# Optimization experiments

Measured on AMD Instinct MI355X. Metric: run time of the kernel, lower is better.

The kernel has to match this reference:

```python
import jax, jax.numpy as jnp
import numpy as np

EMBED = 768
HEADS = 12
HEAD_DIM = EMBED // HEADS
HIDDEN = 4 * EMBED
EPS = 1e-5


def _layernorm(x, g, b):
    mu = jnp.mean(x, axis=-1, keepdims=True)
    var = jnp.var(x, axis=-1, keepdims=True)
    return (x - mu) * jax.lax.rsqrt(var + EPS) * g + b


def setup_inputs() -> dict:
    key = jax.random.key(0)
    ks = jax.random.split(key, 12)
    s_e = 1.0 / np.sqrt(EMBED)
    s_h = 1.0 / np.sqrt(HIDDEN)
    return {
        "x": jax.random.normal(ks[0], (2, 2048, EMBED), dtype=jnp.float32),
        "ln1_g": jnp.ones((EMBED,), jnp.float32),
        "ln1_b": jnp.zeros((EMBED,), jnp.float32),
        "qkv_w": jax.random.uniform(ks[1], (EMBED, 3 * EMBED), jnp.float32, -s_e, s_e),
        "qkv_b": jax.random.uniform(ks[2], (3 * EMBED,), jnp.float32, -s_e, s_e),
        "proj_w": jax.random.uniform(ks[3], (EMBED, EMBED), jnp.float32, -s_e, s_e),
        "proj_b": jax.random.uniform(ks[4], (EMBED,), jnp.float32, -s_e, s_e),
        "ln2_g": jnp.ones((EMBED,), jnp.float32),
        "ln2_b": jnp.zeros((EMBED,), jnp.float32),
        "fc1_w": jax.random.uniform(ks[5], (EMBED, HIDDEN), jnp.float32, -s_e, s_e),
        "fc1_b": jax.random.uniform(ks[6], (HIDDEN,), jnp.float32, -s_e, s_e),
        "fc2_w": jax.random.uniform(ks[7], (HIDDEN, EMBED), jnp.float32, -s_h, s_h),
        "fc2_b": jax.random.uniform(ks[8], (EMBED,), jnp.float32, -s_h, s_h),
    }


def reference(x, ln1_g, ln1_b, qkv_w, qkv_b, proj_w, proj_b,
              ln2_g, ln2_b, fc1_w, fc1_b, fc2_w, fc2_b):
    B, L, C = x.shape
    scale = HEAD_DIM ** -0.5

    # --- attention sublayer (pre-LN) ---
    h = _layernorm(x, ln1_g, ln1_b)
    qkv = h @ qkv_w + qkv_b                       # [B, L, 3C]
    qkv = qkv.reshape(B, L, 3, HEADS, HEAD_DIM)
    q = jnp.transpose(qkv[:, :, 0], (0, 2, 1, 3))  # [B, H, L, D]
    k = jnp.transpose(qkv[:, :, 1], (0, 2, 1, 3))
    v = jnp.transpose(qkv[:, :, 2], (0, 2, 1, 3))
    attn = jnp.einsum('bhqd,bhkd->bhqk', q, k) * scale  # [B, H, L, L]
    attn = jax.nn.softmax(attn, axis=-1)
    out = jnp.einsum('bhqk,bhkd->bhqd', attn, v)  # [B, H, L, D]
    out = jnp.transpose(out, (0, 2, 1, 3)).reshape(B, L, C)
    x = x + (out @ proj_w + proj_b)

    # --- FFN sublayer (pre-LN) ---
    h = _layernorm(x, ln2_g, ln2_b)
    h = jax.nn.gelu(h @ fc1_w + fc1_b, approximate=False)
    x = x + (h @ fc2_w + fc2_b)
    return x
```

## Files before the change

kernel.cpp:

```cpp
#include <hip/hip_runtime.h>
#include <hip/hip_bf16.h>
#include <math.h>

#define EMBED   768
#define NHEADS  12
#define HD      64
#define HIDDEN  3072
#define SEQ     2048
#define BATCH   2
#define ROWS    (BATCH*SEQ)

#define QSCALE  0.1803368801111204f

typedef __bf16 bf16_t;
typedef __attribute__((ext_vector_type(8))) __bf16 bf16x8;
typedef __attribute__((ext_vector_type(4))) __bf16 bf16x4;
typedef __attribute__((ext_vector_type(4))) float f32x4;

static __device__ __forceinline__ f32x4 mfma16(bf16x8 a, bf16x8 b, f32x4 c) {
  return __builtin_amdgcn_mfma_f32_16x16x32_bf16(a, b, c, 0, 0, 0);
}

#if defined(__HIP_DEVICE_COMPILE__) && __has_builtin(__builtin_amdgcn_exp2f)
static __device__ __forceinline__ float fast_exp2(float x) {
  return __builtin_amdgcn_exp2f(x);
}
#else
static __device__ __forceinline__ float fast_exp2(float x) { return exp2f(x); }
#endif

#if defined(__HIP_DEVICE_COMPILE__) && __has_builtin(__builtin_amdgcn_rcpf)
static __device__ __forceinline__ float fast_rcp(float x) {
  return __builtin_amdgcn_rcpf(x);
}
#else
static __device__ __forceinline__ float fast_rcp(float x) { return 1.0f / x; }
#endif

typedef __attribute__((address_space(1))) const void gas_void;
typedef __attribute__((address_space(3))) void las_void;
static __device__ __forceinline__ void gll16(const void* g, void* l) {
  __builtin_amdgcn_global_load_lds((gas_void*)g, (las_void*)l, 16, 0, 0);
}

__global__ __launch_bounds__(256) void prep_kernel(
    const float* __restrict__ w0, bf16_t* __restrict__ o0,
    const float* __restrict__ w1, bf16_t* __restrict__ o1,
    const float* __restrict__ w2, bf16_t* __restrict__ o2,
    const float* __restrict__ w3, bf16_t* __restrict__ o3,
    const float* __restrict__ x,  const float* __restrict__ g,
    const float* __restrict__ bt, bf16_t* __restrict__ lnout)
{
  __shared__ float tile[32][33];
  __shared__ float red[8];
  int lin = blockIdx.x;
  if (lin < 6912) {
    const float* in; bf16_t* out; int R, C, bx, by;
    if (lin < 1728)      { in = w0; out = o0; R = 768;  C = 2304; bx = lin % 72; by = lin / 72; }
    else if (lin < 2304) { in = w1; out = o1; R = 768;  C = 768;  lin -= 1728; bx = lin % 24; by = lin / 24; }
    else if (lin < 4608) { in = w2; out = o2; R = 768;  C = 3072; lin -= 2304; bx = lin % 96; by = lin / 96; }
    else                 { in = w3; out = o3; R = 3072; C = 768;  lin -= 4608; bx = lin % 24; by = lin / 24; }
    int c0 = bx * 32, r0 = by * 32;
    int tx = threadIdx.x & 31, ty = threadIdx.x >> 5;
    #pragma unroll
    for (int p = 0; p < 4; ++p) {
      int r = ty + p * 8;
      tile[r][tx] = in[(size_t)(r0 + r) * C + c0 + tx];
    }
    __syncthreads();
    #pragma unroll
    for (int p = 0; p < 4; ++p) {
      int cc = ty + p * 8;
      out[(size_t)(c0 + cc) * R + r0 + tx] = (bf16_t)tile[tx][cc];
    }
    return;
  }
  int row = lin - 6912;
  int tid = threadIdx.x;
  const float* xr = x + (size_t)row * EMBED;
  float v0 = xr[tid], v1 = xr[tid + 256], v2 = xr[tid + 512];
  float s  = v0 + v1 + v2;
  float s2 = v0*v0 + v1*v1 + v2*v2;
  #pragma unroll
  for (int o = 32; o >= 1; o >>= 1) {
    s  += __shfl_xor(s,  o, 64);
    s2 += __shfl_xor(s2, o, 64);
  }
  int wave = tid >> 6, lane = tid & 63;
  if (lane == 0) { red[wave] = s; red[wave + 4] = s2; }
  __syncthreads();
  s  = red[0] + red[1] + red[2] + red[3];
  s2 = red[4] + red[5] + red[6] + red[7];
  float mu  = s * (1.0f / EMBED);
  float var = s2 * (1.0f / EMBED) - mu * mu;
  float rs  = rsqrtf(var + 1e-5f);
  bf16_t* orow = lnout + (size_t)row * EMBED;
  orow[tid]       = (bf16_t)((v0 - mu) * rs * g[tid]       + bt[tid]);
  orow[tid + 256] = (bf16_t)((v1 - mu) * rs * g[tid + 256] + bt[tid + 256]);
  orow[tid + 512] = (bf16_t)((v2 - mu) * rs * g[tid + 512] + bt[tid + 512]);
}

__global__ __launch_bounds__(256) void ln_kernel(
    const float* __restrict__ x, const float* __restrict__ g,
    const float* __restrict__ bt, bf16_t* __restrict__ out)
{
  int row = blockIdx.x;
  int tid = threadIdx.x;
  const float* xr = x + (size_t)row * EMBED;
  float v0 = xr[tid], v1 = xr[tid + 256], v2 = xr[tid + 512];
  float s  = v0 + v1 + v2;
  float s2 = v0*v0 + v1*v1 + v2*v2;
  #pragma unroll
  for (int o = 32; o >= 1; o >>= 1) {
    s  += __shfl_xor(s,  o, 64);
    s2 += __shfl_xor(s2, o, 64);
  }
  __shared__ float red[8];
  int wave = tid >> 6, lane = tid & 63;
  if (lane == 0) { red[wave] = s; red[wave + 4] = s2; }
  __syncthreads();
  s  = red[0] + red[1] + red[2] + red[3];
  s2 = red[4] + red[5] + red[6] + red[7];
  float mu  = s * (1.0f / EMBED);
  float var = s2 * (1.0f / EMBED) - mu * mu;
  float rs  = rsqrtf(var + 1e-5f);
  bf16_t* orow = out + (size_t)row * EMBED;
  orow[tid]       = (bf16_t)((v0 - mu) * rs * g[tid]       + bt[tid]);
  orow[tid + 256] = (bf16_t)((v1 - mu) * rs * g[tid + 256] + bt[tid + 256]);
  orow[tid + 512] = (bf16_t)((v2 - mu) * rs * g[tid + 512] + bt[tid + 512]);
}

template<int MODE, int BN, int SK = 1>
__global__ __launch_bounds__(256) void gemm_kernel(
    const bf16_t* __restrict__ A, const bf16_t* __restrict__ WT,
    const float* __restrict__ bias, const float* __restrict__ res,
    void* __restrict__ outp, bf16_t* __restrict__ vt, int N, int K)
{
  constexpr int JT = BN / 32;
  __shared__ bf16_t As[128 * 64];
  __shared__ bf16_t Bs[BN * 64];
  int tid = threadIdx.x;
  int lane = tid & 63, wave = tid >> 6;
  int l15 = lane & 15, quad = lane >> 4;
  int wm = wave >> 1, wn = wave & 1;

  int Nn = N / BN;
  int lin = blockIdx.x;
  int kslice = 0, k_lo = 0, k_hi = K;
  if (MODE == 4) {
    kslice = lin % SK; lin /= SK;
    k_lo = kslice * (K / SK); k_hi = k_lo + K / SK;
  }
  int bm = (lin & 7) + 8 * ((lin >> 3) / Nn);
  int bn = (lin >> 3) % Nn;
  int m0 = bm * 128, n0 = bn * BN;

  f32x4 acc[4][JT];
  #pragma unroll
  for (int i = 0; i < 4; ++i)
    #pragma unroll
    for (int j = 0; j < JT; ++j)
      acc[i][j] = (f32x4){0.f, 0.f, 0.f, 0.f};

  int grow = lane >> 3;
  int gcol = ((lane & 7) ^ grow) * 8;
  const bf16_t* abase = A  + (size_t)(m0 + wave * 32 + grow) * K + gcol;
  const bf16_t* bbase = WT + (size_t)(n0 + wave * (BN / 4) + grow) * K + gcol;
  int swk = l15 & 7;

  for (int k0 = k_lo; k0 < k_hi; k0 += 64) {
    #pragma unroll
    for (int a = 0; a < 4; ++a)
      gll16(abase + (size_t)a * 8 * K + k0, &As[(wave * 32 + a * 8) * 64]);
    #pragma unroll
    for (int a = 0; a < BN / 32; ++a)
      gll16(bbase + (size_t)a * 8 * K + k0, &Bs[(wave * (BN / 4) + a * 8) * 64]);
    __syncthreads();

    #pragma unroll
    for (int g = 0; g < 2; ++g) {
      bf16x8 af[4], bfr[JT];
      #pragma unroll
      for (int i = 0; i < 4; ++i)
        af[i] = *(const bf16x8*)
            &As[(wm * 64 + i * 16 + l15) * 64 + (((g * 4 + quad) ^ swk) * 8)];
      #pragma unroll
      for (int j = 0; j < JT; ++j)
        bfr[j] = *(const bf16x8*)
            &Bs[(wn * (BN / 2) + j * 16 + l15) * 64 + (((g * 4 + quad) ^ swk) * 8)];
      #pragma unroll
      for (int i = 0; i < 4; ++i)
        #pragma unroll
        for (int j = 0; j < JT; ++j)
          acc[i][j] = mfma16(af[i], bfr[j], acc[i][j]);
    }
    __syncthreads();
  }

  #pragma unroll
  for (int i = 0; i < 4; ++i) {
    int mbase = m0 + wm * 64 + i * 16 + quad * 4;
    #pragma unroll
    for (int j = 0; j < JT; ++j) {
      int n = n0 + wn * (BN / 2) + j * 16 + l15;
      float bn_ = (MODE == 4 && kslice != 0) ? 0.f : bias[n];
      if (MODE == 3 && n >= 1536) {
        int dcol = n - 1536;
        int hh = dcol >> 6, dd = dcol & 63;
        int bsel = mbase >> 11, l = mbase & 2047;
        union { bf16_t b4[4]; uint2 u; } pk;
        #pragma unroll
        for (int r = 0; r < 4; ++r)
          pk.b4[r] = (bf16_t)(acc[i][j][r] + bn_);
        *(uint2*)&vt[(((size_t)bsel * NHEADS + hh) * HD + dd) * SEQ + l] = pk.u;
        continue;
      }
      #pragma unroll
      for (int r = 0; r < 4; ++r) {
        size_t idx = (size_t)(mbase + r) * N + n;
        float v = acc[i][j][r] + bn_;
        if (MODE == 1) {
          float e = fast_exp2(fminf(v * (2.3020807f + 0.10293776f * v * v), 120.f));
          v = v * e * fast_rcp(e + 1.0f);
        }
        if (MODE == 3 && n < 768) v *= QSCALE;
        if (MODE == 2) {
          v += res[idx];
          ((float*)outp)[idx] = v;
        } else if (MODE == 4) {
          atomicAdd((float*)outp + idx, v);
        } else {
          ((bf16_t*)outp)[idx] = (bf16_t)v;
        }
      }
    }
  }
}

__global__ __launch_bounds__(256, 3) void attn_kernel(
    const bf16_t* __restrict__ qkv, const bf16_t* __restrict__ vt,
    bf16_t* __restrict__ attnout)
{
  __attribute__((aligned(16))) __shared__ bf16_t smem[4 * 3 * 2048];
  __shared__ float dsumf[4][64];

  int qt = blockIdx.x, h = blockIdx.y, b = blockIdx.z;
  int tid = threadIdx.x;
  int wave = tid >> 6, lane = tid & 63;
  int l15 = lane & 15, quad = lane >> 4;
  int q0 = qt * 64;
  int bh = b * NHEADS + h;

  bf16_t* wbase = smem + wave * 3 * 2048;

  bf16x8 bq[4][2];
  #pragma unroll
  for (int qi = 0; qi < 4; ++qi) {
    const bf16_t* qrow = qkv + (size_t)(b * SEQ + q0 + qi * 16 + l15) * 2304
                             + h * HD + quad * 8;
    bq[qi][0] = *(const bf16x8*)qrow;
    bq[qi][1] = *(const bf16x8*)(qrow + 32);
  }
  __asm__ volatile("s_waitcnt vmcnt(0)" ::: "memory");

  f32x4 accO[4][4];
  f32x4 accL[4];
  #pragma unroll
  for (int qi = 0; qi < 4; ++qi) {
    accL[qi] = (f32x4){0.f, 0.f, 0.f, 0.f};
    #pragma unroll
    for (int t2 = 0; t2 < 4; ++t2)
      accO[qi][t2] = (f32x4){0.f, 0.f, 0.f, 0.f};
  }

  bf16x8 ones;
  #pragma unroll
  for (int r = 0; r < 8; ++r) ones[r] = (bf16_t)1.0f;

  int krow_l = lane >> 3;
  int kchunk = ((lane & 7) ^ krow_l) * 8;
  const bf16_t* ksrc0 = qkv + (size_t)(b * SEQ + wave * 16 + krow_l) * 2304
                            + 768 + h * HD + kchunk;
  int vrow_l = lane >> 1;
  int vchunk = ((lane & 1) ^ ((vrow_l >> 2) & 1)) * 8;
  const bf16_t* vsrc0 = vt + ((size_t)bh * HD + vrow_l) * SEQ + wave * 16 + vchunk;

  constexpr int NIT = SEQ / 64;

  auto stage = [&](int t) {
    bf16_t* kb = wbase + (t % 3) * 2048;
    bf16_t* vb = kb + 1024;
    const bf16_t* ks = ksrc0 + (size_t)(t * 64) * 2304;
    const bf16_t* vs = vsrc0 + t * 64;
    #pragma unroll
    for (int p = 0; p < 2; ++p) {
      gll16(ks + (size_t)(p * 8) * 2304, kb + p * 512);
      gll16(vs + (size_t)(p * 32) * SEQ, vb + p * 512);
    }
  };

  stage(0);
  stage(1);

  int vphys = (((quad >> 1) ^ ((l15 >> 2) & 1)) * 8) + (quad & 1) * 4;

  for (int p = 0; p < NIT / 2; ++p) {
    int ta = 2 * p, tb = 2 * p + 1;
    __asm__ volatile("s_waitcnt vmcnt(0)" ::: "memory");

    const bf16_t* kba = wbase + (ta % 3) * 2048;
    const bf16_t* vba = kba + 1024;
    const bf16_t* kbb = wbase + (tb % 3) * 2048;
    const bf16_t* vbb = kbb + 1024;

    bf16x8 aka[2], akb[2];
    #pragma unroll
    for (int f = 0; f < 2; ++f) {
      int koff = (((f * 4 + quad) ^ (l15 & 7)) * 8);
      aka[f] = *(const bf16x8*)&kba[l15 * 64 + koff];
      akb[f] = *(const bf16x8*)&kbb[l15 * 64 + koff];
    }

    bf16x8 bv8[4];
    #pragma unroll
    for (int t2 = 0; t2 < 4; ++t2) {
      bf16x4 lo = *(const bf16x4*)&vba[(t2 * 16 + l15) * 16 + vphys];
      bf16x4 hi = *(const bf16x4*)&vbb[(t2 * 16 + l15) * 16 + vphys];
      bf16x8 c;
      #pragma unroll
      for (int r = 0; r < 4; ++r) { c[r] = lo[r]; c[r + 4] = hi[r]; }
      bv8[t2] = c;
    }

    __asm__ volatile("s_waitcnt lgkmcnt(0)" ::: "memory");
    if (p < NIT / 2 - 1) {
      stage(2 * p + 2);
      stage(2 * p + 3);
    }

    #pragma unroll
    for (int qi = 0; qi < 4; ++qi) {
      f32x4 sa = (f32x4){0.f, 0.f, 0.f, 0.f};
      sa = mfma16(aka[0], bq[qi][0], sa);
      sa = mfma16(aka[1], bq[qi][1], sa);
      f32x4 sb = (f32x4){0.f, 0.f, 0.f, 0.f};
      sb = mfma16(akb[0], bq[qi][0], sb);
      sb = mfma16(akb[1], bq[qi][1], sb);
      bf16x8 ap;
      #pragma unroll
      for (int r = 0; r < 4; ++r) {
        ap[r]     = (bf16_t)fast_exp2(sa[r]);
        ap[r + 4] = (bf16_t)fast_exp2(sb[r]);
      }
      accL[qi] = mfma16(ap, ones, accL[qi]);
      #pragma unroll
      for (int t2 = 0; t2 < 4; ++t2)
        accO[qi][t2] = mfma16(ap, bv8[t2], accO[qi][t2]);
    }
  }

  if (l15 == 0) {
    #pragma unroll
    for (int qi = 0; qi < 4; ++qi)
      #pragma unroll
      for (int r = 0; r < 4; ++r)
        dsumf[wave][qi * 16 + quad * 4 + r] = accL[qi][r];
  }
  __syncthreads();

  float* slabf = (float*)smem;

  for (int pass = 0; pass < 2; ++pass) {
    #pragma unroll
    for (int qi2 = 0; qi2 < 2; ++qi2) {
      int qi = pass * 2 + qi2;
      #pragma unroll
      for (int t2 = 0; t2 < 4; ++t2)
        #pragma unroll
        for (int r = 0; r < 4; ++r)
          slabf[wave * 2048 + (qi2 * 16 + quad * 4 + r) * 64 + t2 * 16 + l15]
              = accO[qi][t2][r];
    }
    __syncthreads();
    int row = tid >> 3;
    int d0 = (tid & 7) * 8;
    f32x4 o0 = (f32x4){0.f,0.f,0.f,0.f}, o1 = (f32x4){0.f,0.f,0.f,0.f};
    #pragma unroll
    for (int sw = 0; sw < 4; ++sw) {
      o0 += *(const f32x4*)&slabf[sw * 2048 + row * 64 + d0];
      o1 += *(const f32x4*)&slabf[sw * 2048 + row * 64 + d0 + 4];
    }
    int q_abs = pass * 32 + row;
    float den = dsumf[0][q_abs] + dsumf[1][q_abs] + dsumf[2][q_abs] + dsumf[3][q_abs];
    float inv = 1.0f / den;
    bf16_t ob[8];
    #pragma unroll
    for (int j = 0; j < 4; ++j) {
      ob[j]     = (bf16_t)(o0[j] * inv);
      ob[j + 4] = (bf16_t)(o1[j] * inv);
    }
    *(uint4*)&attnout[(size_t)(b * SEQ + q0 + q_abs) * EMBED + h * HD + d0]
        = *(const uint4*)ob;
    if (pass == 0) __syncthreads();
  }
}

extern "C" void kernel_launch(void* const* d_in, const int* in_sizes, int n_in,
                              void* d_out, int out_size, void* d_ws, size_t ws_size,
                              hipStream_t stream) {
  (void)in_sizes; (void)n_in; (void)out_size; (void)ws_size;
  const float* x      = (const float*)d_in[0];
  const float* ln1_g  = (const float*)d_in[1];
  const float* ln1_b  = (const float*)d_in[2];
  const float* qkv_w  = (const float*)d_in[3];
  const float* qkv_b  = (const float*)d_in[4];
  const float* proj_w = (const float*)d_in[5];
  const float* proj_b = (const float*)d_in[6];
  const float* ln2_g  = (const float*)d_in[7];
  const float* ln2_b  = (const float*)d_in[8];
  const float* fc1_w  = (const float*)d_in[9];
  const float* fc1_b  = (const float*)d_in[10];
  const float* fc2_w  = (const float*)d_in[11];
  const float* fc2_b  = (const float*)d_in[12];
  float* out = (float*)d_out;

  char* p = (char*)d_ws;
  bf16_t* wqkvT  = (bf16_t*)p; p += (size_t)2304 * 768 * 2;
  bf16_t* wprojT = (bf16_t*)p; p += (size_t)768 * 768 * 2;
  bf16_t* wfc1T  = (bf16_t*)p; p += (size_t)3072 * 768 * 2;
  bf16_t* wfc2T  = (bf16_t*)p; p += (size_t)768 * 3072 * 2;
  bf16_t* hbuf   = (bf16_t*)p; p += (size_t)ROWS * 768 * 2;
  bf16_t* qkv    = (bf16_t*)p;
  bf16_t* hid    = (bf16_t*)p; p += (size_t)ROWS * 3072 * 2;
  bf16_t* vt     = (bf16_t*)p; p += (size_t)BATCH * NHEADS * HD * SEQ * 2;
  bf16_t* attno  = (bf16_t*)p; p += (size_t)ROWS * 768 * 2;

  prep_kernel<<<6912 + ROWS, 256, 0, stream>>>(
      qkv_w, wqkvT, proj_w, wprojT, fc1_w, wfc1T, fc2_w, wfc2T,
      x, ln1_g, ln1_b, hbuf);

  gemm_kernel<3,128><<<32 * (2304/128), 256, 0, stream>>>(
      hbuf, wqkvT, qkv_b, nullptr, qkv, vt, 2304, 768);
  attn_kernel<<<dim3(SEQ/64, NHEADS, BATCH), 256, 0, stream>>>(qkv, vt, attno);
  gemm_kernel<2,64><<<32 * (768/64), 256, 0, stream>>>(
      attno, wprojT, proj_b, x, out, nullptr, 768, 768);

  ln_kernel<<<ROWS, 256, 0, stream>>>(out, ln2_g, ln2_b, hbuf);
  gemm_kernel<1,128><<<32 * (3072/128), 256, 0, stream>>>(
      hbuf, wfc1T, fc1_b, nullptr, hid, nullptr, 3072, 768);
  gemm_kernel<4,128,4><<<4 * 32 * (768/128), 256, 0, stream>>>(
      hid, wfc2T, fc2_b, nullptr, out, nullptr, 768, 3072);
}
```

Baseline: 274.4 us.

## Double-buffer GEMM LDS tiles with async prefetch and retune fc2 split-K

The GEMM kernel now uses two LDS buffers and issues global-to-LDS loads for the next K step before computing on the current one. Partial vmcnt waits and raw barriers replace the two __syncthreads per iteration, so load latency can overlap MFMA work. The fc2 launch also changes from BN=128 with split-K 4 to BN=64 with split-K 2. This doubles LDS use per block, which may lower occupancy, and the hand-counted vmcnt values must match the number of outstanding loads to stay correct.

```diff
diff --git a/kernel.cpp b/kernel.cpp
--- a/kernel.cpp
+++ b/kernel.cpp
@@ -137,8 +137,8 @@
     void* __restrict__ outp, bf16_t* __restrict__ vt, int N, int K)
 {
   constexpr int JT = BN / 32;
-  __shared__ bf16_t As[128 * 64];
-  __shared__ bf16_t Bs[BN * 64];
+  __shared__ bf16_t As[2 * 128 * 64];
+  __shared__ bf16_t Bs[2 * BN * 64];
   int tid = threadIdx.x;
   int lane = tid & 63, wave = tid >> 6;
   int l15 = lane & 15, quad = lane >> 4;
@@ -168,33 +168,54 @@
   const bf16_t* bbase = WT + (size_t)(n0 + wave * (BN / 4) + grow) * K + gcol;
   int swk = l15 & 7;
 
-  for (int k0 = k_lo; k0 < k_hi; k0 += 64) {
+  auto stageg = [&](int k0, int buf) {
+    bf16_t* asp = &As[buf * (128 * 64)];
+    bf16_t* bsp = &Bs[buf * (BN * 64)];
     #pragma unroll
     for (int a = 0; a < 4; ++a)
-      gll16(abase + (size_t)a * 8 * K + k0, &As[(wave * 32 + a * 8) * 64]);
+      gll16(abase + (size_t)a * 8 * K + k0, &asp[(wave * 32 + a * 8) * 64]);
     #pragma unroll
     for (int a = 0; a < BN / 32; ++a)
-      gll16(bbase + (size_t)a * 8 * K + k0, &Bs[(wave * (BN / 4) + a * 8) * 64]);
-    __syncthreads();
-
+      gll16(bbase + (size_t)a * 8 * K + k0, &bsp[(wave * (BN / 4) + a * 8) * 64]);
+  };
+
+  int nsteps = (k_hi - k_lo) / 64;
+  stageg(k_lo, 0);
+
+  for (int t = 0; t < nsteps; ++t) {
+    if (t + 1 < nsteps) {
+      stageg(k_lo + (t + 1) * 64, (t + 1) & 1);
+      if constexpr (BN == 128)
+        __asm__ volatile("s_waitcnt vmcnt(8)" ::: "memory");
+      else
+        __asm__ volatile("s_waitcnt vmcnt(6)" ::: "memory");
+    } else {
+      __asm__ volatile("s_waitcnt vmcnt(0)" ::: "memory");
+    }
+    __builtin_amdgcn_s_barrier();
+    __builtin_amdgcn_sched_barrier(0);
+
+    const bf16_t* asp = &As[(t & 1) * (128 * 64)];
+    const bf16_t* bsp = &Bs[(t & 1) * (BN * 64)];
     #pragma unroll
     for (int g = 0; g < 2; ++g) {
       bf16x8 af[4], bfr[JT];
       #pragma unroll
       for (int i = 0; i < 4; ++i)
         af[i] = *(const bf16x8*)
-            &As[(wm * 64 + i * 16 + l15) * 64 + (((g * 4 + quad) ^ swk) * 8)];
+            &asp[(wm * 64 + i * 16 + l15) * 64 + (((g * 4 + quad) ^ swk) * 8)];
       #pragma unroll
       for (int j = 0; j < JT; ++j)
         bfr[j] = *(const bf16x8*)
-            &Bs[(wn * (BN / 2) + j * 16 + l15) * 64 + (((g * 4 + quad) ^ swk) * 8)];
+            &bsp[(wn * (BN / 2) + j * 16 + l15) * 64 + (((g * 4 + quad) ^ swk) * 8)];
       #pragma unroll
       for (int i = 0; i < 4; ++i)
         #pragma unroll
         for (int j = 0; j < JT; ++j)
           acc[i][j] = mfma16(af[i], bfr[j], acc[i][j]);
     }
-    __syncthreads();
+    __asm__ volatile("s_waitcnt lgkmcnt(0)" ::: "memory");
+    __builtin_amdgcn_s_barrier();
   }
 
   #pragma unroll
@@ -448,6 +469,6 @@
   ln_kernel<<<ROWS, 256, 0, stream>>>(out, ln2_g, ln2_b, hbuf);
   gemm_kernel<1,128><<<32 * (3072/128), 256, 0, stream>>>(
       hbuf, wfc1T, fc1_b, nullptr, hid, nullptr, 3072, 768);
-  gemm_kernel<4,128,4><<<4 * 32 * (768/128), 256, 0, stream>>>(
+  gemm_kernel<4,64,2><<<2 * 32 * (768/64), 256, 0, stream>>>(
       hid, wfc2T, fc2_b, nullptr, out, nullptr, 768, 3072);
 }
```

Result: faster. 267.8 us (-2.4%).
